# Kernel tuning notes

Measured on AMD Instinct MI355X. Metric: run time of the kernel, lower is better.

## Reference

```python
import jax, jax.numpy as jnp
import numpy as np

VOCAB = 100000
EMBED = 64
B, S, K = 1024, 50, 20


def setup_inputs() -> dict:
    key = jax.random.key(0)
    k1, k2, k3 = jax.random.split(key, 3)
    content_input = jax.random.randint(k1, (B, S, K), 0, VOCAB)
    # nn.Linear(vocab_size, embed_size): weight [E, V], bias [E]
    W = jax.random.normal(k2, (EMBED, VOCAB), dtype=jnp.float32) * 0.02
    b = jax.random.normal(k3, (EMBED,), dtype=jnp.float32) * 0.02
    return {"content_input": content_input, "W": W, "b": b}


def reference(content_input, W, b):
    # Original: multi_hot = one_hot(ids, V).sum(2); out = multi_hot @ W.T + b
    # Mathematically identical gather-reduce: sum rows of W.T at ids, plus bias.
    # Duplicate ids are correctly counted because the one-hot sum accumulates counts.
    rows = jnp.take(W.T, content_input, axis=0)  # [B, S, K, E]
    return rows.sum(axis=2) + b                  # [B, S, E]
```

## Files before the change

### kernel.cpp

```cpp
#include <hip/hip_runtime.h>
#include <hip/hip_bf16.h>

#define VOCAB 100000
#define EMBED 64
#define NPAIR (1024 * 50)
#define KIDS  20

typedef int   int4v   __attribute__((ext_vector_type(4)));
typedef float float2v __attribute__((ext_vector_type(2)));

static __device__ inline ushort f2bf(float f) {
    __hip_bfloat16 h = __float2bfloat16(f);
    return __builtin_bit_cast(ushort, h);
}
static __device__ inline float bf2f(ushort u) {
    unsigned int v = ((unsigned int)u) << 16;
    return __builtin_bit_cast(float, v);
}

__global__ __launch_bounds__(256) void convert_w(const float* __restrict__ W,
                                                 ushort* __restrict__ Wt) {
    __shared__ float tile[64][65];
    const int v0 = blockIdx.x * 64;
    const int tx = threadIdx.x & 63;
    const int ty = threadIdx.x >> 6;
    const int v = v0 + tx;
    if (v < VOCAB) {
        #pragma unroll
        for (int e = ty; e < 64; e += 4) {
            tile[tx][e] = __builtin_nontemporal_load(&W[(size_t)e * VOCAB + v]);
        }
    }
    __syncthreads();
    const int r  = threadIdx.x >> 2;
    const int c0 = (threadIdx.x & 3) * 16;
    if (v0 + r < VOCAB) {
        uint pk[8];
        #pragma unroll
        for (int i = 0; i < 8; i++) {
            ushort lo = f2bf(tile[r][c0 + 2 * i + 0]);
            ushort hi = f2bf(tile[r][c0 + 2 * i + 1]);
            pk[i] = (uint)lo | ((uint)hi << 16);
        }
        uint4* outv = (uint4*)(Wt + (size_t)(v0 + r) * 64 + c0);
        outv[0] = make_uint4(pk[0], pk[1], pk[2], pk[3]);
        outv[1] = make_uint4(pk[4], pk[5], pk[6], pk[7]);
    }
}

__global__ __launch_bounds__(256) void gather_bf16(const int* __restrict__ ids,
                                                   const uint* __restrict__ Wt32,
                                                   const float* __restrict__ bias,
                                                   float* __restrict__ out) {
    const int pp   = (blockIdx.x * blockDim.x + threadIdx.x) >> 6;
    const int lane = threadIdx.x & 63;
    if (pp >= NPAIR / 2) return;

    const int h    = lane >> 5;
    const int ll   = lane & 31;
    const int pair = pp * 2 + h;

    const int4v* idv = (const int4v*)(ids + (size_t)pair * KIDS);

    float accE = 0.f, accO = 0.f;
    #pragma unroll
    for (int k = 0; k < 5; k++) {
        int4v q = idv[k];
        uint u0 = Wt32[(((uint)q.x) << 5) + ll];
        uint u1 = Wt32[(((uint)q.y) << 5) + ll];
        uint u2 = Wt32[(((uint)q.z) << 5) + ll];
        uint u3 = Wt32[(((uint)q.w) << 5) + ll];
        accE += bf2f((ushort)(u0 & 0xffff)); accO += bf2f((ushort)(u0 >> 16));
        accE += bf2f((ushort)(u1 & 0xffff)); accO += bf2f((ushort)(u1 >> 16));
        accE += bf2f((ushort)(u2 & 0xffff)); accO += bf2f((ushort)(u2 >> 16));
        accE += bf2f((ushort)(u3 & 0xffff)); accO += bf2f((ushort)(u3 >> 16));
    }

    float2v bb = ((const float2v*)bias)[ll];
    float2v r;
    r.x = accE + bb.x;
    r.y = accO + bb.y;
    __builtin_nontemporal_store(r, &((float2v*)out)[(size_t)pair * 32 + ll]);
}

__global__ __launch_bounds__(256) void gather_direct(const int* __restrict__ ids,
                                                     const float* __restrict__ W,
                                                     const float* __restrict__ bias,
                                                     float* __restrict__ out) {
    const int wave = (blockIdx.x * blockDim.x + threadIdx.x) >> 6;
    const int lane = threadIdx.x & 63;
    if (wave >= NPAIR) return;

    const int* myids = ids + (size_t)wave * KIDS;
    float acc = bias[lane];
    #pragma unroll
    for (int k = 0; k < KIDS; k++) {
        int id = myids[k];
        acc += W[(size_t)lane * VOCAB + id];
    }
    out[(size_t)wave * 64 + lane] = acc;
}

extern "C" void kernel_launch(void* const* d_in, const int* in_sizes, int n_in,
                              void* d_out, int out_size, void* d_ws, size_t ws_size,
                              hipStream_t stream) {
    const int*   ids  = (const int*)d_in[0];
    const float* W    = (const float*)d_in[1];
    const float* bias = (const float*)d_in[2];
    float*       out  = (float*)d_out;

    const size_t wt_bytes = (size_t)VOCAB * EMBED * sizeof(ushort);

    if (ws_size >= wt_bytes) {
        ushort* Wt = (ushort*)d_ws;
        const int tr_blocks = (VOCAB + 63) / 64;
        convert_w<<<tr_blocks, 256, 0, stream>>>(W, Wt);
        const int g_blocks = ((NPAIR / 2) * 64 + 255) / 256;
        gather_bf16<<<g_blocks, 256, 0, stream>>>(ids, (const uint*)Wt, bias, out);
    } else {
        const int g_blocks = (NPAIR * 64 + 255) / 256;
        gather_direct<<<g_blocks, 256, 0, stream>>>(ids, W, bias, out);
    }
}
```

Baseline: 103.4 us.

## Slice bf16 table into four column slabs and pin slabs to XCD pairs

The converted bf16 table is stored as four separate 16-column slabs instead of one row-major table. The gather kernel assigns each block to an XCD, chosen by block index modulo 8, so that each pair of XCDs only touches one 3.2MB slab. That slab can then fit in the XCD-local L2 and cut HBM and Infinity Fabric traffic for the random row gathers. In exchange each gather is a 32-byte row fragment read by 16 lanes with ushort loads, and the ids are re-read four times, once per slab.

```diff
diff --git a/kernel.cpp b/kernel.cpp
--- a/kernel.cpp
+++ b/kernel.cpp
@@ -7,7 +7,6 @@
 #define KIDS  20
 
 typedef int   int4v   __attribute__((ext_vector_type(4)));
-typedef float float2v __attribute__((ext_vector_type(2)));
 
 static __device__ inline ushort f2bf(float f) {
     __hip_bfloat16 h = __float2bfloat16(f);
@@ -42,45 +41,42 @@
             ushort hi = f2bf(tile[r][c0 + 2 * i + 1]);
             pk[i] = (uint)lo | ((uint)hi << 16);
         }
-        uint4* outv = (uint4*)(Wt + (size_t)(v0 + r) * 64 + c0);
+        ushort* dst = Wt + (size_t)(c0 >> 4) * VOCAB * 16 + (size_t)(v0 + r) * 16;
+        uint4* outv = (uint4*)dst;
         outv[0] = make_uint4(pk[0], pk[1], pk[2], pk[3]);
         outv[1] = make_uint4(pk[4], pk[5], pk[6], pk[7]);
     }
 }
 
-__global__ __launch_bounds__(256) void gather_bf16(const int* __restrict__ ids,
-                                                   const uint* __restrict__ Wt32,
-                                                   const float* __restrict__ bias,
-                                                   float* __restrict__ out) {
-    const int pp   = (blockIdx.x * blockDim.x + threadIdx.x) >> 6;
-    const int lane = threadIdx.x & 63;
-    if (pp >= NPAIR / 2) return;
+__global__ __launch_bounds__(256) void gather_sliced(const int* __restrict__ ids,
+                                                     const ushort* __restrict__ Wt,
+                                                     const float* __restrict__ bias,
+                                                     float* __restrict__ out) {
+    const int b    = blockIdx.x;
+    const int xcd  = b & 7;
+    const int xi   = b >> 3;
+    const int s    = xcd >> 1;
+    const int half = xcd & 1;
+    const int wv   = (int)(threadIdx.x >> 6);
+    const int lane = (int)(threadIdx.x & 63);
+    const int g    = lane >> 4;
+    const int d    = lane & 15;
 
-    const int h    = lane >> 5;
-    const int ll   = lane & 31;
-    const int pair = pp * 2 + h;
+    const int pair = half * (NPAIR / 2) + xi * 16 + wv * 4 + g;
+    const ushort* tbl = Wt + (size_t)s * VOCAB * 16;
 
     const int4v* idv = (const int4v*)(ids + (size_t)pair * KIDS);
-
-    float accE = 0.f, accO = 0.f;
+    float acc = 0.f;
     #pragma unroll
     for (int k = 0; k < 5; k++) {
-        int4v q = idv[k];
-        uint u0 = Wt32[(((uint)q.x) << 5) + ll];
-        uint u1 = Wt32[(((uint)q.y) << 5) + ll];
-        uint u2 = Wt32[(((uint)q.z) << 5) + ll];
-        uint u3 = Wt32[(((uint)q.w) << 5) + ll];
-        accE += bf2f((ushort)(u0 & 0xffff)); accO += bf2f((ushort)(u0 >> 16));
-        accE += bf2f((ushort)(u1 & 0xffff)); accO += bf2f((ushort)(u1 >> 16));
-        accE += bf2f((ushort)(u2 & 0xffff)); accO += bf2f((ushort)(u2 >> 16));
-        accE += bf2f((ushort)(u3 & 0xffff)); accO += bf2f((ushort)(u3 >> 16));
+        int4v q = __builtin_nontemporal_load(&idv[k]);
+        acc += bf2f(tbl[(((uint)q.x) << 4) + d]);
+        acc += bf2f(tbl[(((uint)q.y) << 4) + d]);
+        acc += bf2f(tbl[(((uint)q.z) << 4) + d]);
+        acc += bf2f(tbl[(((uint)q.w) << 4) + d]);
     }
-
-    float2v bb = ((const float2v*)bias)[ll];
-    float2v r;
-    r.x = accE + bb.x;
-    r.y = accO + bb.y;
-    __builtin_nontemporal_store(r, &((float2v*)out)[(size_t)pair * 32 + ll]);
+    acc += bias[s * 16 + d];
+    __builtin_nontemporal_store(acc, &out[(size_t)pair * 64 + s * 16 + d]);
 }
 
 __global__ __launch_bounds__(256) void gather_direct(const int* __restrict__ ids,
@@ -115,8 +111,7 @@
         ushort* Wt = (ushort*)d_ws;
         const int tr_blocks = (VOCAB + 63) / 64;
         convert_w<<<tr_blocks, 256, 0, stream>>>(W, Wt);
-        const int g_blocks = ((NPAIR / 2) * 64 + 255) / 256;
-        gather_bf16<<<g_blocks, 256, 0, stream>>>(ids, (const uint*)Wt, bias, out);
+        gather_sliced<<<12800, 256, 0, stream>>>(ids, Wt, bias, out);
     } else {
         const int g_blocks = (NPAIR * 64 + 255) / 256;
         gather_direct<<<g_blocks, 256, 0, stream>>>(ids, W, bias, out);
```

Measured after the change: 126.2 us. +22.1%, slower.
